# Optimization experiments

Measured on AMD Instinct MI355X. Metric: run time of the kernel, lower is better.

## Reference

```python
import jax, jax.numpy as jnp
import numpy as np

N, F, B = 16384, 1024, 512


def setup_inputs() -> dict:
    key = jax.random.key(0)
    k1, k2, k3, k4, k5 = jax.random.split(key, 5)
    s = 1.0 / np.sqrt(F + B)
    return {
        "behavior": jax.random.normal(k1, (N, B), dtype=jnp.float32),
        "h_prev": jax.random.normal(k2, (N, F), dtype=jnp.float32),
        "c_prev": jax.random.normal(k3, (N, F), dtype=jnp.float32),
        "Wh": jax.random.normal(k4, (4 * F, F), dtype=jnp.float32) * s,
        "Wx": jax.random.normal(k5, (4 * F, B), dtype=jnp.float32) * s,
        "b": jnp.zeros((4 * F,), dtype=jnp.float32),
    }


def reference(behavior, h_prev, c_prev, Wh, Wx, b):
    # Fused single GEMM for all 4 gates: [n, 4F]
    gates = jnp.einsum("nf,gf->ng", h_prev, Wh) + jnp.einsum("nb,gb->ng", behavior, Wx) + b
    i, f, g, o = jnp.split(gates, 4, axis=-1)
    i = jax.nn.sigmoid(i)
    f = jax.nn.sigmoid(f)
    g = jnp.tanh(g)
    o = jax.nn.sigmoid(o)
    c = f * c_prev + i * g
    h = o * jnp.tanh(c)
    return h
```

## Files before the change

### kernel.cpp

```cpp
#include <hip/hip_runtime.h>
#include <hip/hip_bf16.h>
#include <stdint.h>

#define N_ROWS 16384
#define F_DIM  1024
#define B_DIM  512
#define K_DIM  1536
#define G_DIM  4096

typedef __bf16 v8bf __attribute__((ext_vector_type(8)));
typedef float  v4f  __attribute__((ext_vector_type(4)));

typedef const void __attribute__((address_space(1)))* gptr1;
typedef void       __attribute__((address_space(3)))* lptr3;

__device__ __forceinline__ unsigned short f2bf(float x) {
    union { float f; unsigned int u; } c; c.f = x;
    unsigned int u = c.u;
    return (unsigned short)((u + 0x7FFFu + ((u >> 16) & 1u)) >> 16);
}

__global__ void pack_x(const float* __restrict__ behavior,
                       const float* __restrict__ h_prev,
                       unsigned short* __restrict__ A) {
    const int row = blockIdx.x;
    const int col = threadIdx.x * 8;
    const float* src = (col < F_DIM)
        ? h_prev   + (long)row * F_DIM + col
        : behavior + (long)row * B_DIM + (col - F_DIM);
    float4 lo = *(const float4*)src;
    float4 hi = *(const float4*)(src + 4);
    union { unsigned short u[8]; int4 v; } p;
    p.u[0] = f2bf(lo.x); p.u[1] = f2bf(lo.y); p.u[2] = f2bf(lo.z); p.u[3] = f2bf(lo.w);
    p.u[4] = f2bf(hi.x); p.u[5] = f2bf(hi.y); p.u[6] = f2bf(hi.z); p.u[7] = f2bf(hi.w);
    *(int4*)(A + (long)row * K_DIM + col) = p.v;
}

__global__ void pack_w(const float* __restrict__ Wh,
                       const float* __restrict__ Wx,
                       const float* __restrict__ b,
                       unsigned short* __restrict__ W,
                       float* __restrict__ bperm) {
    const int gp   = blockIdx.x;
    const int gate = gp & 3;
    const int f    = gp >> 2;
    const int g    = gate * F_DIM + f;
    const int col  = threadIdx.x * 8;
    const float* src = (col < F_DIM)
        ? Wh + (long)g * F_DIM + col
        : Wx + (long)g * B_DIM + (col - F_DIM);
    float4 lo = *(const float4*)src;
    float4 hi = *(const float4*)(src + 4);
    union { unsigned short u[8]; int4 v; } p;
    p.u[0] = f2bf(lo.x); p.u[1] = f2bf(lo.y); p.u[2] = f2bf(lo.z); p.u[3] = f2bf(lo.w);
    p.u[4] = f2bf(hi.x); p.u[5] = f2bf(hi.y); p.u[6] = f2bf(hi.z); p.u[7] = f2bf(hi.w);
    *(int4*)(W + (long)gp * K_DIM + col) = p.v;
    if (threadIdx.x == 0) bperm[gp] = b[g];
}

__device__ __forceinline__ float sigmoidf_fast(float x) {
    return 1.f / (1.f + __expf(-x));
}
__device__ __forceinline__ float tanhf_fast(float x) {
    return 1.f - 2.f / (__expf(2.f * x) + 1.f);
}

__global__ __launch_bounds__(256, 2) void lstm_gemm(
    const unsigned short* __restrict__ A,
    const unsigned short* __restrict__ W,
    const float* __restrict__ bperm,
    const float* __restrict__ c_prev,
    float* __restrict__ out)
{
    __shared__ unsigned short lds[16384];

    const int m0   = blockIdx.y * 128;
    const int n0   = blockIdx.x * 128;
    const int tid  = threadIdx.x;
    const int lane = tid & 63;
    const int wave = tid >> 6;
    const int wm   = (wave >> 1) * 64;
    const int wn   = (wave & 1) * 64;
    const int lrow = lane & 15;
    const int quad = lane >> 4;

    v4f acc[4][4] = {};

    const int ls_row = lane >> 3;
    const int ls_col = (lane & 7) * 8;
    const unsigned short* a_g = A + (long)(m0 + wave * 32 + ls_row) * K_DIM + ls_col;
    const unsigned short* w_g = W + (long)(n0 + wave * 32 + ls_row) * K_DIM + ls_col;
    unsigned short* a_l = &lds[(wave * 32) * 64];
    unsigned short* w_l = &lds[8192 + (wave * 32) * 64];

    for (int k0 = 0; k0 < K_DIM; k0 += 64) {
#pragma unroll
        for (int c = 0; c < 4; ++c) {
            __builtin_amdgcn_global_load_lds((gptr1)(a_g + (long)c * 8 * K_DIM + k0),
                                             (lptr3)(a_l + c * 8 * 64), 16, 0, 0);
            __builtin_amdgcn_global_load_lds((gptr1)(w_g + (long)c * 8 * K_DIM + k0),
                                             (lptr3)(w_l + c * 8 * 64), 16, 0, 0);
        }
        __syncthreads();

#pragma unroll
        for (int kk = 0; kk < 64; kk += 32) {
            v8bf af[4], bf[4];
#pragma unroll
            for (int mt = 0; mt < 4; ++mt)
                af[mt] = *(const v8bf*)&lds[(wm + mt * 16 + lrow) * 64 + kk + quad * 8];
#pragma unroll
            for (int nt = 0; nt < 4; ++nt)
                bf[nt] = *(const v8bf*)&lds[8192 + (wn + nt * 16 + lrow) * 64 + kk + quad * 8];
#pragma unroll
            for (int mt = 0; mt < 4; ++mt)
#pragma unroll
                for (int nt = 0; nt < 4; ++nt)
                    acc[mt][nt] = __builtin_amdgcn_mfma_f32_16x16x32_bf16(
                        af[mt], bf[nt], acc[mt][nt], 0, 0, 0);
        }
        __syncthreads();
    }

    const int l3 = lane & 3;
    const int fl = (lane & 15) >> 2;
#pragma unroll
    for (int nt = 0; nt < 4; ++nt) {
        const int   gcol = n0 + wn + nt * 16 + lrow;
        const float bias = bperm[gcol];
#pragma unroll
        for (int mt = 0; mt < 4; ++mt) {
            float a0 = acc[mt][nt][0] + bias;
            float a1 = acc[mt][nt][1] + bias;
            float a2 = acc[mt][nt][2] + bias;
            float a3 = acc[mt][nt][3] + bias;
            float s0 = (lane & 1) ? a0 : a1;
            float s1 = (lane & 1) ? a2 : a3;
            float r0 = __shfl_xor(s0, 1, 64);
            float r1 = __shfl_xor(s1, 1, 64);
            if (lane & 1) { a0 = r0; a2 = r1; } else { a1 = r0; a3 = r1; }
            s0 = (lane & 2) ? a0 : a2;
            s1 = (lane & 2) ? a1 : a3;
            r0 = __shfl_xor(s0, 2, 64);
            r1 = __shfl_xor(s1, 2, 64);
            if (lane & 2) { a0 = r0; a1 = r1; } else { a2 = r0; a3 = r1; }
            const float iv = sigmoidf_fast(a0);
            const float fv = sigmoidf_fast(a1);
            const float gv = tanhf_fast(a2);
            const float ov = sigmoidf_fast(a3);
            const int grow = m0 + wm + mt * 16 + quad * 4 + l3;
            const int gf   = ((n0 + wn + nt * 16) >> 2) + fl;
            const float cp = c_prev[(long)grow * F_DIM + gf];
            const float cv = fv * cp + iv * gv;
            const float hv = ov * tanhf_fast(cv);
            out[(long)grow * F_DIM + gf] = hv;
        }
    }
}

extern "C" void kernel_launch(void* const* d_in, const int* in_sizes, int n_in,
                              void* d_out, int out_size, void* d_ws, size_t ws_size,
                              hipStream_t stream) {
    const float* behavior = (const float*)d_in[0];
    const float* h_prev   = (const float*)d_in[1];
    const float* c_prev   = (const float*)d_in[2];
    const float* Wh       = (const float*)d_in[3];
    const float* Wx       = (const float*)d_in[4];
    const float* b        = (const float*)d_in[5];
    float* out = (float*)d_out;

    unsigned short* A  = (unsigned short*)d_ws;
    unsigned short* W  = A + (size_t)N_ROWS * K_DIM;
    float*       bperm = (float*)(W + (size_t)G_DIM * K_DIM);

    pack_x<<<N_ROWS, 192, 0, stream>>>(behavior, h_prev, A);
    pack_w<<<G_DIM, 192, 0, stream>>>(Wh, Wx, b, W, bperm);
    lstm_gemm<<<dim3(G_DIM / 128, N_ROWS / 128), 256, 0, stream>>>(A, W, bperm, c_prev, out);
}
```

Before: 442.3 us.

## XOR-swizzle LDS tiles and stage c_prev/out through LDS for coalesced epilogue

Applies an XOR swizzle to the 16-byte chunk index when global_load_lds fills the A and W tiles, with matching swizzled reads for the MFMA fragments, to cut LDS bank conflicts. The epilogue now loads the block's 128x32 c_prev tile into padded LDS using coalesced float4 reads. Results are written back into that buffer and stored to out with coalesced float4 writes, replacing scattered 4-byte global accesses. This adds two extra block barriers and reuses the GEMM LDS for the staging buffer.

```diff
diff --git a/kernel.cpp b/kernel.cpp
--- a/kernel.cpp
+++ b/kernel.cpp
@@ -7,6 +7,7 @@
 #define B_DIM  512
 #define K_DIM  1536
 #define G_DIM  4096
+#define CB_STR 36
 
 typedef __bf16 v8bf __attribute__((ext_vector_type(8)));
 typedef float  v4f  __attribute__((ext_vector_type(4)));
@@ -83,13 +84,14 @@
     const int wn   = (wave & 1) * 64;
     const int lrow = lane & 15;
     const int quad = lane >> 4;
+    const int r7   = lrow & 7;
 
     v4f acc[4][4] = {};
 
     const int ls_row = lane >> 3;
-    const int ls_col = (lane & 7) * 8;
-    const unsigned short* a_g = A + (long)(m0 + wave * 32 + ls_row) * K_DIM + ls_col;
-    const unsigned short* w_g = W + (long)(n0 + wave * 32 + ls_row) * K_DIM + ls_col;
+    const int ls_blk = (lane & 7) ^ ls_row;
+    const unsigned short* a_g = A + (long)(m0 + wave * 32 + ls_row) * K_DIM + ls_blk * 8;
+    const unsigned short* w_g = W + (long)(n0 + wave * 32 + ls_row) * K_DIM + ls_blk * 8;
     unsigned short* a_l = &lds[(wave * 32) * 64];
     unsigned short* w_l = &lds[8192 + (wave * 32) * 64];
 
@@ -105,13 +107,15 @@
 
 #pragma unroll
         for (int kk = 0; kk < 64; kk += 32) {
+            const int ko = kk >> 3;
+            const int sa = (((quad + ko) ^ r7) * 8);
             v8bf af[4], bf[4];
 #pragma unroll
             for (int mt = 0; mt < 4; ++mt)
-                af[mt] = *(const v8bf*)&lds[(wm + mt * 16 + lrow) * 64 + kk + quad * 8];
+                af[mt] = *(const v8bf*)&lds[(wm + mt * 16 + lrow) * 64 + sa];
 #pragma unroll
             for (int nt = 0; nt < 4; ++nt)
-                bf[nt] = *(const v8bf*)&lds[8192 + (wn + nt * 16 + lrow) * 64 + kk + quad * 8];
+                bf[nt] = *(const v8bf*)&lds[8192 + (wn + nt * 16 + lrow) * 64 + sa];
 #pragma unroll
             for (int mt = 0; mt < 4; ++mt)
 #pragma unroll
@@ -121,6 +125,18 @@
         }
         __syncthreads();
     }
+
+    float* cbuf = (float*)lds;
+    const int fbase = n0 >> 2;
+#pragma unroll
+    for (int i = 0; i < 4; ++i) {
+        const int q  = i * 256 + tid;
+        const int r  = q >> 3;
+        const int c4 = (q & 7) * 4;
+        *(float4*)&cbuf[r * CB_STR + c4] =
+            *(const float4*)&c_prev[(long)(m0 + r) * F_DIM + fbase + c4];
+    }
+    __syncthreads();
 
     const int l3 = lane & 3;
     const int fl = (lane & 15) >> 2;
@@ -148,13 +164,22 @@
             const float fv = sigmoidf_fast(a1);
             const float gv = tanhf_fast(a2);
             const float ov = sigmoidf_fast(a3);
-            const int grow = m0 + wm + mt * 16 + quad * 4 + l3;
-            const int gf   = ((n0 + wn + nt * 16) >> 2) + fl;
-            const float cp = c_prev[(long)grow * F_DIM + gf];
+            const int lr = wm + mt * 16 + quad * 4 + l3;
+            const int lc = ((wn + nt * 16) >> 2) + fl;
+            const float cp = cbuf[lr * CB_STR + lc];
             const float cv = fv * cp + iv * gv;
-            const float hv = ov * tanhf_fast(cv);
-            out[(long)grow * F_DIM + gf] = hv;
+            cbuf[lr * CB_STR + lc] = ov * tanhf_fast(cv);
         }
+    }
+    __syncthreads();
+
+#pragma unroll
+    for (int i = 0; i < 4; ++i) {
+        const int q  = i * 256 + tid;
+        const int r  = q >> 3;
+        const int c4 = (q & 7) * 4;
+        *(float4*)&out[(long)(m0 + r) * F_DIM + fbase + c4] =
+            *(const float4*)&cbuf[r * CB_STR + c4];
     }
 }
 
```

New measurement: 405.1 us. 1.09x faster.
